# Kernel tuning notes

Measured on AMD Instinct MI355X. Metric: run time of the kernel, lower is better.

The kernel has to match this reference:

```python
import jax, jax.numpy as jnp
import numpy as np

# irreps_in1 = 128x0e + 128x1o  (dim 512)
# irreps_in2 = 1x0e + 1x1o     (dim 4)
# irreps_out = 128x0e + 128x1o (dim 512)
MUL = 128
IN1_SEGS = [(128, 0, 0), (128, 1, 128)]   # (mul, l, flat offset)
IN2_SEGS = [(1, 0, 0), (1, 1, 1)]
OUT_SEGS = [(128, 0), (128, 1)]           # (mul, l); offsets 0, 128
# instructions: (i_in1, i_in2, i_out), all mode 'uvu', has_weight, path_weight=1.0
INSTRS = [(0, 0, 0), (0, 1, 1), (1, 0, 1), (1, 1, 0), (1, 1, 1)]
W_PER_INS = 128  # uvu weight numel = mul_in1 * mul_in2 = 128*1
N_EDGES = 131072


def w3j(l1, l2, l3):
    """Real Wigner-3j / CG coefficients for l <= 1, shape (2l1+1, 2l2+1, 2l3+1)."""
    key = (l1, l2, l3)
    if key == (0, 0, 0):
        return jnp.ones((1, 1, 1), jnp.float32)
    inv_sqrt3 = np.float32(1.0 / np.sqrt(3.0))
    if key == (0, 1, 1):
        return (jnp.eye(3, dtype=jnp.float32) * inv_sqrt3).reshape(1, 3, 3)
    if key == (1, 0, 1):
        return (jnp.eye(3, dtype=jnp.float32) * inv_sqrt3).reshape(3, 1, 3)
    if key == (1, 1, 0):
        return (jnp.eye(3, dtype=jnp.float32) * inv_sqrt3).reshape(3, 3, 1)
    if key == (1, 1, 1):
        eps = np.zeros((3, 3, 3), np.float32)
        for i, j, k in [(0, 1, 2), (1, 2, 0), (2, 0, 1)]:
            eps[i, j, k] = 1.0
            eps[i, k, j] = -1.0
        return jnp.asarray(eps / np.sqrt(6.0))
    raise ValueError(key)


def tensor_product(x1, x2, weights):
    n = x1.shape[0]
    out = [jnp.zeros((n, mul, 2 * l + 1), x1.dtype) for mul, l in OUT_SEGS]
    for idx, (i1, i2, io) in enumerate(INSTRS):
        mul1, l1, o1 = IN1_SEGS[i1]
        mul2, l2, o2 = IN2_SEGS[i2]
        l3 = OUT_SEGS[io][1]
        s1 = x1[:, o1:o1 + mul1 * (2 * l1 + 1)].reshape(n, mul1, 2 * l1 + 1)
        s2 = x2[:, o2:o2 + mul2 * (2 * l2 + 1)].reshape(n, mul2, 2 * l2 + 1)
        w = weights[:, idx * W_PER_INS:(idx + 1) * W_PER_INS].reshape(n, mul1, mul2)
        C = w3j(l1, l2, l3).astype(x1.dtype)
        # uvu mode: out[z,u,k] = sum_{v,i,j} C[i,j,k] x1[z,u,i] x2[z,v,j] w[z,u,v]
        res = jnp.einsum('ijk,zui,zvj,zuv->zuk', C, s1, s2, w)
        out[io] = out[io] + res  # path_weight = 1.0
    return jnp.concatenate([o.reshape(n, -1) for o in out], axis=1)


def setup_inputs() -> dict:
    key = jax.random.key(0)
    k1, k2, k3 = jax.random.split(key, 3)
    x1 = jax.random.normal(k1, (N_EDGES, 512), jnp.float32)
    x2 = jax.random.normal(k2, (N_EDGES, 4), jnp.float32)
    weights = jax.random.normal(k3, (N_EDGES, 5 * W_PER_INS), jnp.float32)
    return {"x1": x1, "x2": x2, "weights": weights}


def reference(x1, x2, weights):
    return tensor_product(x1, x2, weights)
```

## Files before the change

### kernel.cpp

```cpp
#include <hip/hip_runtime.h>


typedef float f32x4 __attribute__((ext_vector_type(4)));

__global__ __launch_bounds__(256) void tp_uvu_kernel(
    const float* __restrict__ x1,
    const float* __restrict__ x2,
    const float* __restrict__ w,
    float* __restrict__ out,
    int n_edges)
{
    const int tid = blockIdx.x * blockDim.x + threadIdx.x;
    const int z = tid >> 5;
    const int g = tid & 31;
    if (z >= n_edges) return;

    constexpr float inv_sqrt3 = 0.57735026918962576f;
    constexpr float inv_sqrt6 = 0.40824829046386302f;

    const float* x1row  = x1  + (size_t)z * 512;
    const float* wrow   = w   + (size_t)z * 640;
    float*       outrow = out + (size_t)z * 512;

    const f32x4 x2v = *reinterpret_cast<const f32x4*>(x2 + (size_t)z * 4);
    const f32x4 s4  = *reinterpret_cast<const f32x4*>(x1row + 4 * g);
    const f32x4 va  = *reinterpret_cast<const f32x4*>(x1row + 128 + 12 * g);
    const f32x4 vb  = *reinterpret_cast<const f32x4*>(x1row + 128 + 12 * g + 4);
    const f32x4 vc  = *reinterpret_cast<const f32x4*>(x1row + 128 + 12 * g + 8);
    const f32x4 w0  = *reinterpret_cast<const f32x4*>(wrow +   0 + 4 * g);
    const f32x4 w1  = *reinterpret_cast<const f32x4*>(wrow + 128 + 4 * g);
    const f32x4 w2  = *reinterpret_cast<const f32x4*>(wrow + 256 + 4 * g);
    const f32x4 w3  = *reinterpret_cast<const f32x4*>(wrow + 384 + 4 * g);
    const f32x4 w4  = *reinterpret_cast<const f32x4*>(wrow + 512 + 4 * g);

    __builtin_amdgcn_sched_barrier(0);

    const float a  = x2v.x;
    const float bx = x2v.y, by = x2v.z, bz = x2v.w;

    const float s[4]   = {s4.x, s4.y, s4.z, s4.w};
    const float vv[12] = {va.x, va.y, va.z, va.w,
                          vb.x, vb.y, vb.z, vb.w,
                          vc.x, vc.y, vc.z, vc.w};
    const float W0[4]  = {w0.x, w0.y, w0.z, w0.w};
    const float W1[4]  = {w1.x, w1.y, w1.z, w1.w};
    const float W2[4]  = {w2.x, w2.y, w2.z, w2.w};
    const float W3[4]  = {w3.x, w3.y, w3.z, w3.w};
    const float W4[4]  = {w4.x, w4.y, w4.z, w4.w};

    float os[4];
    float ov[12];
#pragma unroll
    for (int c = 0; c < 4; ++c) {
        const float vx = vv[3 * c + 0];
        const float vy = vv[3 * c + 1];
        const float vz = vv[3 * c + 2];
        const float dot = vx * bx + vy * by + vz * bz;
        os[c] = s[c] * a * W0[c] + inv_sqrt3 * dot * W3[c];

        const float cx = vy * bz - vz * by;
        const float cy = vz * bx - vx * bz;
        const float cz = vx * by - vy * bx;

        const float t1 = inv_sqrt3 * s[c] * W1[c];
        const float t2 = inv_sqrt3 * a   * W2[c];
        const float t4 = inv_sqrt6 * W4[c];
        ov[3 * c + 0] = t1 * bx + t2 * vx + t4 * cx;
        ov[3 * c + 1] = t1 * by + t2 * vy + t4 * cy;
        ov[3 * c + 2] = t1 * bz + t2 * vz + t4 * cz;
    }

    f32x4 o0 = {os[0], os[1], os[2], os[3]};
    f32x4 o1 = {ov[0], ov[1], ov[2], ov[3]};
    f32x4 o2 = {ov[4], ov[5], ov[6], ov[7]};
    f32x4 o3 = {ov[8], ov[9], ov[10], ov[11]};
    *reinterpret_cast<f32x4*>(outrow + 4 * g)            = o0;
    *reinterpret_cast<f32x4*>(outrow + 128 + 12 * g)     = o1;
    *reinterpret_cast<f32x4*>(outrow + 128 + 12 * g + 4) = o2;
    *reinterpret_cast<f32x4*>(outrow + 128 + 12 * g + 8) = o3;
}

extern "C" void kernel_launch(void* const* d_in, const int* in_sizes, int n_in,
                              void* d_out, int out_size, void* d_ws, size_t ws_size,
                              hipStream_t stream) {
    const float* x1 = (const float*)d_in[0];
    const float* x2 = (const float*)d_in[1];
    const float* w  = (const float*)d_in[2];
    float* out = (float*)d_out;

    const int n_edges = in_sizes[0] / 512;
    const long long total_threads = (long long)n_edges * 32;
    const int block = 256;
    const int grid = (int)((total_threads + block - 1) / block);

    tp_uvu_kernel<<<grid, block, 0, stream>>>(x1, x2, w, out, n_edges);
}
```

Before: 156.6 us.

## Process multiple edges per block with double-buffered register prefetch

Each block now handles 64 edges over 8 iterations. Two register tiles are used so that the loads for the next edge group are issued before the current group is computed and stored. The goal is to overlap memory latency with compute in this bandwidth-bound kernel and to reduce the grid size. The cost is higher register pressure and fewer resident waves, which could lower occupancy-based latency hiding.

```diff
diff --git a/kernel.cpp b/kernel.cpp
--- a/kernel.cpp
+++ b/kernel.cpp
@@ -3,50 +3,51 @@
 
 typedef float f32x4 __attribute__((ext_vector_type(4)));
 
-__global__ __launch_bounds__(256) void tp_uvu_kernel(
-    const float* __restrict__ x1,
-    const float* __restrict__ x2,
-    const float* __restrict__ w,
-    float* __restrict__ out,
-    int n_edges)
+struct Tile {
+    f32x4 x2v, s4, va, vb, vc, w0, w1, w2, w3, w4;
+};
+
+__device__ __forceinline__ void load_tile(Tile& T,
+                                          const float* __restrict__ x1,
+                                          const float* __restrict__ x2,
+                                          const float* __restrict__ w,
+                                          int z, int g)
 {
-    const int tid = blockIdx.x * blockDim.x + threadIdx.x;
-    const int z = tid >> 5;
-    const int g = tid & 31;
-    if (z >= n_edges) return;
+    const float* x1row = x1 + (size_t)z * 512;
+    const float* wrow  = w  + (size_t)z * 640;
+    T.x2v = *reinterpret_cast<const f32x4*>(x2 + (size_t)z * 4);
+    T.s4  = *reinterpret_cast<const f32x4*>(x1row + 4 * g);
+    T.va  = *reinterpret_cast<const f32x4*>(x1row + 128 + 12 * g);
+    T.vb  = *reinterpret_cast<const f32x4*>(x1row + 128 + 12 * g + 4);
+    T.vc  = *reinterpret_cast<const f32x4*>(x1row + 128 + 12 * g + 8);
+    T.w0  = *reinterpret_cast<const f32x4*>(wrow +   0 + 4 * g);
+    T.w1  = *reinterpret_cast<const f32x4*>(wrow + 128 + 4 * g);
+    T.w2  = *reinterpret_cast<const f32x4*>(wrow + 256 + 4 * g);
+    T.w3  = *reinterpret_cast<const f32x4*>(wrow + 384 + 4 * g);
+    T.w4  = *reinterpret_cast<const f32x4*>(wrow + 512 + 4 * g);
+}
 
+__device__ __forceinline__ void process_tile(const Tile& T,
+                                             float* __restrict__ out,
+                                             int z, int g)
+{
     constexpr float inv_sqrt3 = 0.57735026918962576f;
     constexpr float inv_sqrt6 = 0.40824829046386302f;
 
-    const float* x1row  = x1  + (size_t)z * 512;
-    const float* wrow   = w   + (size_t)z * 640;
-    float*       outrow = out + (size_t)z * 512;
+    float* outrow = out + (size_t)z * 512;
 
-    const f32x4 x2v = *reinterpret_cast<const f32x4*>(x2 + (size_t)z * 4);
-    const f32x4 s4  = *reinterpret_cast<const f32x4*>(x1row + 4 * g);
-    const f32x4 va  = *reinterpret_cast<const f32x4*>(x1row + 128 + 12 * g);
-    const f32x4 vb  = *reinterpret_cast<const f32x4*>(x1row + 128 + 12 * g + 4);
-    const f32x4 vc  = *reinterpret_cast<const f32x4*>(x1row + 128 + 12 * g + 8);
-    const f32x4 w0  = *reinterpret_cast<const f32x4*>(wrow +   0 + 4 * g);
-    const f32x4 w1  = *reinterpret_cast<const f32x4*>(wrow + 128 + 4 * g);
-    const f32x4 w2  = *reinterpret_cast<const f32x4*>(wrow + 256 + 4 * g);
-    const f32x4 w3  = *reinterpret_cast<const f32x4*>(wrow + 384 + 4 * g);
-    const f32x4 w4  = *reinterpret_cast<const f32x4*>(wrow + 512 + 4 * g);
+    const float a  = T.x2v.x;
+    const float bx = T.x2v.y, by = T.x2v.z, bz = T.x2v.w;
 
-    __builtin_amdgcn_sched_barrier(0);
-
-    const float a  = x2v.x;
-    const float bx = x2v.y, by = x2v.z, bz = x2v.w;
-
-    const float s[4]   = {s4.x, s4.y, s4.z, s4.w};
-    const float vv[12] = {va.x, va.y, va.z, va.w,
-                          vb.x, vb.y, vb.z, vb.w,
-                          vc.x, vc.y, vc.z, vc.w};
-    const float W0[4]  = {w0.x, w0.y, w0.z, w0.w};
-    const float W1[4]  = {w1.x, w1.y, w1.z, w1.w};
-    const float W2[4]  = {w2.x, w2.y, w2.z, w2.w};
-    const float W3[4]  = {w3.x, w3.y, w3.z, w3.w};
-    const float W4[4]  = {w4.x, w4.y, w4.z, w4.w};
+    const float s[4]   = {T.s4.x, T.s4.y, T.s4.z, T.s4.w};
+    const float vv[12] = {T.va.x, T.va.y, T.va.z, T.va.w,
+                          T.vb.x, T.vb.y, T.vb.z, T.vb.w,
+                          T.vc.x, T.vc.y, T.vc.z, T.vc.w};
+    const float W0[4]  = {T.w0.x, T.w0.y, T.w0.z, T.w0.w};
+    const float W1[4]  = {T.w1.x, T.w1.y, T.w1.z, T.w1.w};
+    const float W2[4]  = {T.w2.x, T.w2.y, T.w2.z, T.w2.w};
+    const float W3[4]  = {T.w3.x, T.w3.y, T.w3.z, T.w3.w};
+    const float W4[4]  = {T.w4.x, T.w4.y, T.w4.z, T.w4.w};
 
     float os[4];
     float ov[12];
@@ -80,6 +81,41 @@
     *reinterpret_cast<f32x4*>(outrow + 128 + 12 * g + 8) = o3;
 }
 
+#define EDGES_PER_ITER 8
+#define ITERS 8
+
+__global__ __launch_bounds__(256) void tp_uvu_kernel(
+    const float* __restrict__ x1,
+    const float* __restrict__ x2,
+    const float* __restrict__ w,
+    float* __restrict__ out,
+    int n_edges)
+{
+    const int g    = threadIdx.x & 31;
+    const int eoff = threadIdx.x >> 5;
+    const int base = blockIdx.x * (EDGES_PER_ITER * ITERS);
+    const int z0   = base + eoff;
+    const int lim  = min(n_edges, base + EDGES_PER_ITER * ITERS);
+
+    Tile A, B;
+    if (z0 < lim) load_tile(A, x1, x2, w, z0, g);
+
+#pragma unroll
+    for (int i = 0; i < 4; ++i) {
+        const int zA = z0 + 2 * EDGES_PER_ITER * i;
+        const int zB = zA + EDGES_PER_ITER;
+        const int zA2 = zA + 2 * EDGES_PER_ITER;
+
+        if (zB < lim) load_tile(B, x1, x2, w, zB, g);
+        __builtin_amdgcn_sched_barrier(0);
+        if (zA < lim) process_tile(A, out, zA, g);
+
+        if (zA2 < lim) load_tile(A, x1, x2, w, zA2, g);
+        __builtin_amdgcn_sched_barrier(0);
+        if (zB < lim) process_tile(B, out, zB, g);
+    }
+}
+
 extern "C" void kernel_launch(void* const* d_in, const int* in_sizes, int n_in,
                               void* d_out, int out_size, void* d_ws, size_t ws_size,
                               hipStream_t stream) {
@@ -89,9 +125,8 @@
     float* out = (float*)d_out;
 
     const int n_edges = in_sizes[0] / 512;
-    const long long total_threads = (long long)n_edges * 32;
-    const int block = 256;
-    const int grid = (int)((total_threads + block - 1) / block);
+    const int edges_per_block = EDGES_PER_ITER * ITERS;
+    const int grid = (n_edges + edges_per_block - 1) / edges_per_block;
 
-    tp_uvu_kernel<<<grid, block, 0, stream>>>(x1, x2, w, out, n_edges);
+    tp_uvu_kernel<<<grid, 256, 0, stream>>>(x1, x2, w, out, n_edges);
 }
```

Measured after the change: 205.9 us. 31.5% more time.
